# Kernel tuning notes

Hardware: AMD Instinct MI355X
Metric: run time of the kernel (lower is better)

Reference implementation:

```python
import jax, jax.numpy as jnp
import numpy as np

B, T, V, E, A, H, IMG, ENC = 128, 25, 10000, 512, 512, 512, 14, 2048
P = IMG * IMG  # 196 pixels


def setup_inputs() -> dict:
    key = jax.random.key(0)
    ks = jax.random.split(key, 24)
    w = lambda i, shape: jax.random.normal(ks[i], shape, jnp.float32) * 0.02
    captions = jax.random.randint(ks[0], (B, T), 0, V, dtype=jnp.int32)
    lens = jax.random.randint(ks[1], (B, 1), 5, T + 1, dtype=jnp.int32)
    lens = lens.at[0, 0].set(T)  # guarantee max(captions_lengths) == T (static)
    encoder_out = jax.random.normal(ks[2], (B, IMG, IMG, ENC), jnp.float32)
    return {
        'captions': captions,
        'encoder_out': encoder_out,
        'captions_lengths': lens,
        'emb_W': w(3, (V, E)),
        'att_enc_W': w(4, (A, ENC)), 'att_enc_b': jnp.zeros((A,), jnp.float32),
        'att_dec_W': w(5, (A, E)), 'att_dec_b': jnp.zeros((A,), jnp.float32),
        'att_fin_W': w(6, (1, A)), 'att_fin_b': jnp.zeros((1,), jnp.float32),
        'f_beta_W': w(7, (ENC, H)), 'f_beta_b': jnp.zeros((ENC,), jnp.float32),
        'W_ih': w(8, (4 * H, ENC + E)), 'b_ih': jnp.zeros((4 * H,), jnp.float32),
        'W_hh': w(9, (4 * H, H)), 'b_hh': jnp.zeros((4 * H,), jnp.float32),
        'lin_W': w(10, (V, H)), 'lin_b': jnp.zeros((V,), jnp.float32),
        'h_init_W': w(11, (H, ENC)), 'h_init_b': jnp.zeros((H,), jnp.float32),
        'c_init_W': w(12, (H, ENC)), 'c_init_b': jnp.zeros((H,), jnp.float32),
    }


def reference(captions, encoder_out, captions_lengths, emb_W,
              att_enc_W, att_enc_b, att_dec_W, att_dec_b, att_fin_W, att_fin_b,
              f_beta_W, f_beta_b, W_ih, b_ih, W_hh, b_hh,
              lin_W, lin_b, h_init_W, h_init_b, c_init_W, c_init_b):
    b = encoder_out.shape[0]
    enc = encoder_out.reshape(b, -1, ENC)                 # [B,P,2048]
    lens = captions_lengths[:, 0]
    sort_ind = jnp.argsort(-lens)                         # descending-length sort
    lens_s = lens[sort_ind]
    enc = enc[sort_ind]
    caps = captions[sort_ind]
    emb = emb_W[caps]                                     # [B,T,E]
    enc_mean = enc.mean(axis=1)                           # [B,2048]
    h0 = enc_mean @ h_init_W.T + h_init_b                 # [B,H]
    c0 = enc_mean @ c_init_W.T + c_init_b
    # precompute encoder side of additive attention (loop-invariant)
    att_enc = jnp.einsum('bpe,ae->bpa', enc, att_enc_W) + att_enc_b  # [B,P,A]

    t_steps = caps.shape[1]
    active = (lens_s[None, :] > jnp.arange(1, t_steps)[:, None])     # [T-1,B]
    emb_prev = jnp.swapaxes(emb[:, :t_steps - 1], 0, 1)              # [T-1,B,E]

    def step(carry, xs):
        h, c = carry
        dec, act = xs                                      # [B,E], [B]
        # additive attention
        att_d = dec @ att_dec_W.T + att_dec_b              # [B,A]
        score = jax.nn.relu(att_enc + att_d[:, None, :]) @ att_fin_W[0] + att_fin_b[0]  # [B,P]
        wts = jax.nn.softmax(score, axis=1)
        ctx = jnp.einsum('bpe,bp->be', enc, wts)           # [B,2048]
        gate = jax.nn.sigmoid(h @ f_beta_W.T + f_beta_b)   # [B,2048]
        ctx = gate * ctx
        x = jnp.concatenate([ctx, dec], axis=1)            # [B,2048+E]
        gates = x @ W_ih.T + b_ih + h @ W_hh.T + b_hh      # [B,4H]
        i, f, g, o = jnp.split(gates, 4, axis=1)
        c_new = jax.nn.sigmoid(f) * c + jax.nn.sigmoid(i) * jnp.tanh(g)
        h_new = jax.nn.sigmoid(o) * jnp.tanh(c_new)
        m = act[:, None]
        h = jnp.where(m, h_new, h)                         # finished rows frozen
        c = jnp.where(m, c_new, c)
        logits = h @ lin_W.T + lin_b                       # [B,V]
        y = jnp.where(m, logits, 0.0)                      # unwritten rows stay 0
        return (h, c), y

    (_, _), ys = jax.lax.scan(step, (h0, c0), (emb_prev, active))
    preds = jnp.zeros((b, t_steps, V), jnp.float32)
    preds = preds.at[:, 0, 0].set(1.0)
    preds = preds.at[:, 1:, :].set(jnp.swapaxes(ys, 0, 1))
    return preds, caps, lens_s, sort_ind
```

## Files before the change

### kernel.cpp

```cpp
#include <hip/hip_runtime.h>
#include <hip/hip_cooperative_groups.h>
#include <math.h>

namespace cg = cooperative_groups;

#define Bb 128
#define Tt 25
#define Vv 10000
#define Ee 512
#define Aa 512
#define Hh 512
#define ENCc 2048
#define Pp 196
#define NSTEP 24
#define NPAD 10112
#define NWG 64

#define OUT_CAPS  ((size_t)Bb*Tt*Vv)
#define OUT_LENS  (OUT_CAPS + (size_t)Bb*Tt)
#define OUT_SORT  (OUT_LENS + Bb)

typedef __bf16 bf16x8 __attribute__((ext_vector_type(8)));
typedef __bf16 bf16x4 __attribute__((ext_vector_type(4)));
typedef float  f32x4  __attribute__((ext_vector_type(4)));

__device__ __forceinline__ float sigm(float x) { return 1.0f / (1.0f + expf(-x)); }

__global__ void k_sort(const int* __restrict__ captions, const int* __restrict__ cap_lens,
                       int* sort_ind, int* lens_s, int* caps_s,
                       int* row_emb, int* logit_rowoff, int* logit_mask,
                       float* out)
{
    int b = threadIdx.x;
    __shared__ int lens_sh[Bb];
    int len = cap_lens[b];
    lens_sh[b] = len;
    __syncthreads();
    int r = 0;
    for (int k = 0; k < Bb; k++) {
        int lk = lens_sh[k];
        if (lk > len || (lk == len && k < b)) r++;
    }
    sort_ind[r] = b;
    lens_s[r] = len;
    for (int t = 0; t < Tt; t++) {
        int cv = captions[b * Tt + t];
        caps_s[r * Tt + t] = cv;
        out[OUT_CAPS + (size_t)r * Tt + t] = (float)cv;
    }
    out[OUT_LENS + r] = (float)len;
    out[OUT_SORT + r] = (float)b;
    __syncthreads();
    for (int m = b; m < NSTEP * Bb; m += Bb) {
        int t = m / Bb, bb = m % Bb;
        row_emb[m] = caps_s[bb * Tt + t];
        logit_rowoff[m] = (bb * Tt + (t + 1)) * Vv;
        logit_mask[m] = (lens_s[bb] > t + 1) ? 1 : 0;
    }
}

__global__ void k_preds0(float* out)
{
    size_t i = (size_t)blockIdx.x * 256 + threadIdx.x;
    if (i >= (size_t)Bb * Vv) return;
    size_t b = i / Vv, v = i % Vv;
    out[b * Tt * Vv + v] = (v == 0) ? 1.0f : 0.0f;
}

__global__ void k_bias(const float* b_ih, const float* b_hh,
                       const float* aeb, const float* adb,
                       float* bias2, float* bias_att)
{
    int i = blockIdx.x * 256 + threadIdx.x;
    if (i < 2048) bias2[i] = b_ih[i] + b_hh[i];
    if (i < 512)  bias_att[i] = aeb[i] + adb[i];
}

__global__ void k_cvt_enc(const float* __restrict__ src, const int* __restrict__ sind,
                          __bf16* __restrict__ dst)
{
    int row = blockIdx.y;
    int e4 = blockIdx.x * 256 + threadIdx.x;
    int b = row / Pp, p = row % Pp;
    const float4 v = *(const float4*)(src + ((size_t)(sind[b] * Pp + p)) * ENCc + e4 * 4);
    bf16x4 o = { (__bf16)v.x, (__bf16)v.y, (__bf16)v.z, (__bf16)v.w };
    *(bf16x4*)(dst + (size_t)row * ENCc + e4 * 4) = o;
}

__global__ void k_cvt(const float* __restrict__ src, __bf16* __restrict__ dst, int n4)
{
    int i = blockIdx.x * 256 + threadIdx.x;
    if (i >= n4) return;
    const float4 v = *(const float4*)(src + (size_t)i * 4);
    bf16x4 o = { (__bf16)v.x, (__bf16)v.y, (__bf16)v.z, (__bf16)v.w };
    *(bf16x4*)(dst + (size_t)i * 4) = o;
}

__global__ void k_cvt_lin(const float* __restrict__ src, __bf16* __restrict__ dst)
{
    int i = blockIdx.x * 256 + threadIdx.x;
    if (i >= NPAD * 128) return;
    int row = i >> 7, e = (i & 127) * 4;
    bf16x4 o;
    if (row < Vv) {
        const float4 v = *(const float4*)(src + (size_t)row * Hh + e);
        o = bf16x4{ (__bf16)v.x, (__bf16)v.y, (__bf16)v.z, (__bf16)v.w };
    } else {
        o = bf16x4{ (__bf16)0.f, (__bf16)0.f, (__bf16)0.f, (__bf16)0.f };
    }
    *(bf16x4*)(dst + (size_t)row * Hh + e) = o;
}

__global__ void k_cvt_emb(const float* __restrict__ emb_W, const int* __restrict__ row_emb,
                          __bf16* __restrict__ dst)
{
    int i = blockIdx.x * 256 + threadIdx.x;
    int row = i >> 7, e = (i & 127) * 4;
    const float4 v = *(const float4*)(emb_W + (size_t)row_emb[row] * Ee + e);
    bf16x4 o = { (__bf16)v.x, (__bf16)v.y, (__bf16)v.z, (__bf16)v.w };
    *(bf16x4*)(dst + (size_t)row * Ee + e) = o;
}

__global__ void k_cvt_wihd(const float* __restrict__ W_ih, __bf16* __restrict__ dst)
{
    int i = blockIdx.x * 256 + threadIdx.x;
    int row = i >> 7, e = (i & 127) * 4;
    const float4 v = *(const float4*)(W_ih + (size_t)row * 2560 + 2048 + e);
    bf16x4 o = { (__bf16)v.x, (__bf16)v.y, (__bf16)v.z, (__bf16)v.w };
    *(bf16x4*)(dst + (size_t)row * 512 + e) = o;
}

__global__ void k_wcat2(const float* __restrict__ W_ih, const float* __restrict__ W_hh,
                        __bf16* __restrict__ W2)
{
    int n = blockIdx.y;
    int k4 = blockIdx.x * 256 + threadIdx.x;
    if (k4 >= 640) return;
    int k = k4 * 4;
    float4 v;
    if (k < 2048) v = *(const float4*)(W_ih + (size_t)n * 2560 + k);
    else          v = *(const float4*)(W_hh + (size_t)n * 512 + (k - 2048));
    bf16x4 o = { (__bf16)v.x, (__bf16)v.y, (__bf16)v.z, (__bf16)v.w };
    *(bf16x4*)(W2 + (size_t)n * 2560 + k) = o;
}

__global__ void k_enc_mean(const __bf16* __restrict__ enc, __bf16* __restrict__ emean)
{
    int b = blockIdx.y;
    int e = blockIdx.x * 256 + threadIdx.x;
    const __bf16* base = enc + (size_t)b * Pp * ENCc + e;
    float s = 0.0f;
    for (int p = 0; p < Pp; p++) s += (float)base[(size_t)p * ENCc];
    emean[(size_t)b * ENCc + e] = (__bf16)(s / 196.0f);
}

template<int MODE>
__launch_bounds__(256)
__global__ void mfma_gemm(const __bf16* __restrict__ A, const __bf16* __restrict__ B,
                          const float* __restrict__ bias, void* __restrict__ Cout,
                          int K, int Nout, int Ncol,
                          const int* __restrict__ c_rowoff,
                          const int* __restrict__ mmask,
                          size_t bsA, size_t bsB, size_t bsC)
{
    __shared__ __bf16 sA[128 * 32];
    __shared__ __bf16 sB[128 * 32];
    const int tid = threadIdx.x;
    const int lane = tid & 63;
    const int wave = tid >> 6;
    const int z = blockIdx.z;
    const int m0 = blockIdx.y * 128, n0 = blockIdx.x * 128;
    const int wr = (wave & 1) * 64, wc = (wave >> 1) * 64;
    f32x4 acc[4][4] = {};
    const __bf16* Aptr = A + bsA * z + (size_t)m0 * K;
    const __bf16* Bptr = B + bsB * z + (size_t)n0 * K;
    const int c0 = tid, c1 = tid + 256;
    const int ar0 = c0 >> 2, ak0 = (c0 & 3) * 8;
    const int ar1 = c1 >> 2, ak1 = (c1 & 3) * 8;
    const int kq = (lane >> 4) * 8, mr = lane & 15;

    for (int k0 = 0; k0 < K; k0 += 32) {
        __builtin_amdgcn_global_load_lds(
            (const __attribute__((address_space(1))) void*)(Aptr + (size_t)ar0 * K + k0 + ak0),
            (__attribute__((address_space(3))) void*)(sA + c0 * 8), 16, 0, 0);
        __builtin_amdgcn_global_load_lds(
            (const __attribute__((address_space(1))) void*)(Aptr + (size_t)ar1 * K + k0 + ak1),
            (__attribute__((address_space(3))) void*)(sA + c1 * 8), 16, 0, 0);
        __builtin_amdgcn_global_load_lds(
            (const __attribute__((address_space(1))) void*)(Bptr + (size_t)ar0 * K + k0 + ak0),
            (__attribute__((address_space(3))) void*)(sB + c0 * 8), 16, 0, 0);
        __builtin_amdgcn_global_load_lds(
            (const __attribute__((address_space(1))) void*)(Bptr + (size_t)ar1 * K + k0 + ak1),
            (__attribute__((address_space(3))) void*)(sB + c1 * 8), 16, 0, 0);
        __syncthreads();
        bf16x8 af[4], bfr[4];
        #pragma unroll
        for (int i = 0; i < 4; i++)
            af[i] = *(const bf16x8*)(sA + (wr + i * 16 + mr) * 32 + kq);
        #pragma unroll
        for (int j = 0; j < 4; j++)
            bfr[j] = *(const bf16x8*)(sB + (wc + j * 16 + mr) * 32 + kq);
        #pragma unroll
        for (int i = 0; i < 4; i++)
            #pragma unroll
            for (int j = 0; j < 4; j++)
                acc[i][j] = __builtin_amdgcn_mfma_f32_16x16x32_bf16(af[i], bfr[j], acc[i][j], 0, 0, 0);
        __syncthreads();
    }

    const int rq = (lane >> 4) * 4, cq = lane & 15;
    #pragma unroll
    for (int i = 0; i < 4; i++) {
        #pragma unroll
        for (int j = 0; j < 4; j++) {
            #pragma unroll
            for (int r = 0; r < 4; r++) {
                int row = m0 + wr + i * 16 + rq + r;
                int col = n0 + wc + j * 16 + cq;
                if ((MODE == 1 || MODE == 2) && col >= Ncol) continue;
                float v = acc[i][j][r] + (bias ? bias[col] : 0.0f);
                size_t ro = (c_rowoff ? (size_t)c_rowoff[row] : (size_t)row * Nout) + bsC * z;
                if (MODE == 2) {
                    if (!mmask[row]) v = 0.0f;
                    ((float*)Cout)[ro + col] = v;
                } else if (MODE == 1) {
                    ((__bf16*)Cout)[ro + col] = (__bf16)v;
                } else {
                    ((float*)Cout)[ro + col] = v;
                }
            }
        }
    }
}

__global__ void k_scores(const __bf16* __restrict__ ET, const float* __restrict__ att_d,
                         const float* __restrict__ fin_W, const float* __restrict__ fin_b,
                         float* __restrict__ wts)
{
    __shared__ float Dls[512 * 12];
    const int b = blockIdx.y;
    const int tb = blockIdx.x * 12;
    const int tid = threadIdx.x;
    #pragma unroll
    for (int tt = 0; tt < 12; tt++)
        for (int a = tid; a < 512; a += 256)
            Dls[a * 12 + tt] = att_d[((size_t)(tb + tt) * Bb + b) * Aa + a];
    __syncthreads();
    const int p = tid;
    if (p >= Pp) return;
    float acc[12];
    #pragma unroll
    for (int i = 0; i < 12; i++) acc[i] = 0.0f;
    const __bf16* ep = ET + (size_t)b * Aa * Pp + p;
    for (int a = 0; a < 512; a++) {
        float e = (float)ep[(size_t)a * Pp];
        float fw = fin_W[a];
        const float4* dp = (const float4*)(Dls + a * 12);
        float4 d0 = dp[0], d1 = dp[1], d2 = dp[2];
        acc[0] += fmaxf(e + d0.x, 0.0f) * fw;
        acc[1] += fmaxf(e + d0.y, 0.0f) * fw;
        acc[2] += fmaxf(e + d0.z, 0.0f) * fw;
        acc[3] += fmaxf(e + d0.w, 0.0f) * fw;
        acc[4] += fmaxf(e + d1.x, 0.0f) * fw;
        acc[5] += fmaxf(e + d1.y, 0.0f) * fw;
        acc[6] += fmaxf(e + d1.z, 0.0f) * fw;
        acc[7] += fmaxf(e + d1.w, 0.0f) * fw;
        acc[8] += fmaxf(e + d2.x, 0.0f) * fw;
        acc[9] += fmaxf(e + d2.y, 0.0f) * fw;
        acc[10] += fmaxf(e + d2.z, 0.0f) * fw;
        acc[11] += fmaxf(e + d2.w, 0.0f) * fw;
    }
    float fb = fin_b[0];
    #pragma unroll
    for (int tt = 0; tt < 12; tt++)
        wts[((size_t)(tb + tt) * Bb + b) * Pp + p] = acc[tt] + fb;
}

__global__ void k_softmax(float* scores)
{
    int tb = blockIdx.x;
    float* row = scores + (size_t)tb * Pp;
    int lane = threadIdx.x;
    float v[4];
    float mx = -1e30f;
    #pragma unroll
    for (int i = 0; i < 4; i++) {
        int p = lane + i * 64;
        v[i] = (p < Pp) ? row[p] : -1e30f;
        mx = fmaxf(mx, v[i]);
    }
    #pragma unroll
    for (int off = 32; off > 0; off >>= 1) mx = fmaxf(mx, __shfl_down(mx, off));
    mx = __shfl(mx, 0);
    float s = 0.0f;
    #pragma unroll
    for (int i = 0; i < 4; i++) {
        int p = lane + i * 64;
        v[i] = (p < Pp) ? expf(v[i] - mx) : 0.0f;
        s += v[i];
    }
    #pragma unroll
    for (int off = 32; off > 0; off >>= 1) s += __shfl_down(s, off);
    s = __shfl(s, 0);
    float inv = 1.0f / s;
    #pragma unroll
    for (int i = 0; i < 4; i++) {
        int p = lane + i * 64;
        if (p < Pp) row[p] = v[i] * inv;
    }
}

__global__ void k_ctx(const __bf16* __restrict__ enc, const float* __restrict__ wts,
                      float* __restrict__ ctx_raw)
{
    int b = blockIdx.y;
    int e = blockIdx.x * 256 + threadIdx.x;
    __shared__ float w_s[NSTEP][Pp];
    int tid = threadIdx.x;
    for (int idx = tid; idx < NSTEP * Pp; idx += 256) {
        int t = idx / Pp, p = idx % Pp;
        w_s[t][p] = wts[((size_t)t * Bb + b) * Pp + p];
    }
    __syncthreads();
    const __bf16* base = enc + (size_t)b * Pp * ENCc + e;
    float acc[NSTEP];
    #pragma unroll
    for (int t = 0; t < NSTEP; t++) acc[t] = 0.0f;
    for (int p = 0; p < Pp; p++) {
        float v = (float)base[(size_t)p * ENCc];
        #pragma unroll
        for (int t = 0; t < NSTEP; t++) acc[t] += w_s[t][p] * v;
    }
    for (int t = 0; t < NSTEP; t++)
        ctx_raw[((size_t)t * Bb + b) * ENCc + e] = acc[t];
}

__device__ __forceinline__ bf16x8 lds_frag(const __bf16* s, int row, int g)
{
    int slot = row * 16 + (g ^ (row & 7));
    return *(const bf16x8*)(s + slot * 8);
}

__launch_bounds__(256)
__global__ void k_loop(__bf16* __restrict__ xctx, __bf16* __restrict__ hbuf0,
                       __bf16* __restrict__ hbuf1, float* __restrict__ cbuf,
                       const float* __restrict__ ctx_raw,
                       const __bf16* __restrict__ fbW, const float* __restrict__ fbb,
                       const __bf16* __restrict__ W2, const float* __restrict__ gdec,
                       __bf16* __restrict__ hall, const int* __restrict__ lens)
{
    cg::grid_group grid = cg::this_grid();
    __shared__ __bf16 sA[128 * 128];
    __shared__ __bf16 sB[32 * 128];
    const int tid = threadIdx.x, lane = tid & 63, wave = tid >> 6;
    const int wg = blockIdx.x;
    const int cq = lane & 15, rq4 = (lane >> 4) * 4;
    const int mbase = wave * 32;
    const int kq = lane >> 4;

    for (int t = 0; t < NSTEP; t++) {
        const __bf16* hcur = (t & 1) ? hbuf1 : hbuf0;
        __bf16* hnext = (t & 1) ? hbuf0 : hbuf1;
        {
            const int cb = wg * 32;
            f32x4 acc[2][2] = {};
            for (int k0 = 0; k0 < 512; k0 += 128) {
                #pragma unroll
                for (int i = 0; i < 8; i++) {
                    int flat = tid + 256 * i;
                    int row = flat >> 4, gs = flat & 15;
                    int gsrc = gs ^ (row & 7);
                    __builtin_amdgcn_global_load_lds(
                        (const __attribute__((address_space(1))) void*)(hcur + (size_t)row * 512 + k0 + gsrc * 8),
                        (__attribute__((address_space(3))) void*)(sA + flat * 8), 16, 0, 0);
                }
                #pragma unroll
                for (int i = 0; i < 2; i++) {
                    int flat = tid + 256 * i;
                    int row = flat >> 4, gs = flat & 15;
                    int gsrc = gs ^ (row & 7);
                    __builtin_amdgcn_global_load_lds(
                        (const __attribute__((address_space(1))) void*)(fbW + (size_t)(cb + row) * 512 + k0 + gsrc * 8),
                        (__attribute__((address_space(3))) void*)(sB + flat * 8), 16, 0, 0);
                }
                __syncthreads();
                #pragma unroll
                for (int ks = 0; ks < 4; ks++) {
                    int g = ks * 4 + kq;
                    bf16x8 af[2], bfv[2];
                    #pragma unroll
                    for (int mi = 0; mi < 2; mi++) af[mi] = lds_frag(sA, mbase + mi * 16 + cq, g);
                    #pragma unroll
                    for (int ni = 0; ni < 2; ni++) bfv[ni] = lds_frag(sB, ni * 16 + cq, g);
                    #pragma unroll
                    for (int mi = 0; mi < 2; mi++)
                        #pragma unroll
                        for (int ni = 0; ni < 2; ni++)
                            acc[mi][ni] = __builtin_amdgcn_mfma_f32_16x16x32_bf16(af[mi], bfv[ni], acc[mi][ni], 0, 0, 0);
                }
                __syncthreads();
            }
            const float* cr = ctx_raw + (size_t)t * Bb * ENCc;
            #pragma unroll
            for (int mi = 0; mi < 2; mi++)
                #pragma unroll
                for (int ni = 0; ni < 2; ni++)
                    #pragma unroll
                    for (int r = 0; r < 4; r++) {
                        int row = mbase + mi * 16 + rq4 + r;
                        int col = cb + ni * 16 + cq;
                        float v = acc[mi][ni][r] + fbb[col];
                        float x = sigm(v) * cr[(size_t)row * ENCc + col];
                        xctx[(size_t)row * ENCc + col] = (__bf16)x;
                    }
        }
        grid.sync();
        {
            const int jb = wg * 8;
            f32x4 acc[2][2] = {};
            for (int k0 = 0; k0 < 2560; k0 += 128) {
                const bool inH = (k0 >= 2048);
                #pragma unroll
                for (int i = 0; i < 8; i++) {
                    int flat = tid + 256 * i;
                    int row = flat >> 4, gs = flat & 15;
                    int gsrc = gs ^ (row & 7);
                    const __bf16* src = inH ? (hcur + (size_t)row * 512 + (k0 - 2048) + gsrc * 8)
                                            : (xctx + (size_t)row * ENCc + k0 + gsrc * 8);
                    __builtin_amdgcn_global_load_lds(
                        (const __attribute__((address_space(1))) void*)src,
                        (__attribute__((address_space(3))) void*)(sA + flat * 8), 16, 0, 0);
                }
                #pragma unroll
                for (int i = 0; i < 2; i++) {
                    int flat = tid + 256 * i;
                    int row = flat >> 4, gs = flat & 15;
                    int gsrc = gs ^ (row & 7);
                    int wrow = (row >> 3) * 512 + jb + (row & 7);
                    __builtin_amdgcn_global_load_lds(
                        (const __attribute__((address_space(1))) void*)(W2 + (size_t)wrow * 2560 + k0 + gsrc * 8),
                        (__attribute__((address_space(3))) void*)(sB + flat * 8), 16, 0, 0);
                }
                __syncthreads();
                #pragma unroll
                for (int ks = 0; ks < 4; ks++) {
                    int g = ks * 4 + kq;
                    bf16x8 af[2], bfv[2];
                    #pragma unroll
                    for (int mi = 0; mi < 2; mi++) af[mi] = lds_frag(sA, mbase + mi * 16 + cq, g);
                    #pragma unroll
                    for (int ni = 0; ni < 2; ni++) bfv[ni] = lds_frag(sB, ni * 16 + cq, g);
                    #pragma unroll
                    for (int mi = 0; mi < 2; mi++)
                        #pragma unroll
                        for (int ni = 0; ni < 2; ni++)
                            acc[mi][ni] = __builtin_amdgcn_mfma_f32_16x16x32_bf16(af[mi], bfv[ni], acc[mi][ni], 0, 0, 0);
                }
                __syncthreads();
            }
            const int j = jb + (cq & 7);
            const int g0 = cq >> 3;
            #pragma unroll
            for (int mi = 0; mi < 2; mi++)
                #pragma unroll
                for (int r = 0; r < 4; r++) {
                    int row = mbase + mi * 16 + rq4 + r;
                    size_t gb = (size_t)(t * Bb + row) * 2048;
                    float a0 = acc[mi][0][r] + gdec[gb + (size_t)g0 * 512 + j];
                    float a1 = acc[mi][1][r] + gdec[gb + (size_t)(2 + g0) * 512 + j];
                    float p0 = __shfl_xor(a0, 8);
                    float p1 = __shfl_xor(a1, 8);
                    float iv, fv, gv, ov;
                    if (cq < 8) { iv = a0; gv = a1; fv = p0; ov = p1; }
                    else        { iv = p0; gv = p1; fv = a0; ov = a1; }
                    float co = cbuf[(size_t)row * 512 + j];
                    float cn = sigm(fv) * co + sigm(iv) * tanhf(gv);
                    float hn = sigm(ov) * tanhf(cn);
                    bool act = lens[row] > (t + 1);
                    __bf16 hold = hcur[(size_t)row * 512 + j];
                    __bf16 hv = act ? (__bf16)hn : hold;
                    if (cq < 8) {
                        if (act) cbuf[(size_t)row * 512 + j] = cn;
                        hnext[(size_t)row * 512 + j] = hv;
                        hall[((size_t)t * Bb + row) * 512 + j] = hv;
                    }
                }
        }
        grid.sync();
    }
}

extern "C" void kernel_launch(void* const* d_in, const int* in_sizes, int n_in,
                              void* d_out, int out_size, void* d_ws, size_t ws_size,
                              hipStream_t stream)
{
    const int*   captions    = (const int*)d_in[0];
    const float* encoder_out = (const float*)d_in[1];
    const int*   cap_lens    = (const int*)d_in[2];
    const float* emb_W       = (const float*)d_in[3];
    const float* att_enc_W   = (const float*)d_in[4];
    const float* att_enc_b   = (const float*)d_in[5];
    const float* att_dec_W   = (const float*)d_in[6];
    const float* att_dec_b   = (const float*)d_in[7];
    const float* att_fin_W   = (const float*)d_in[8];
    const float* att_fin_b   = (const float*)d_in[9];
    const float* f_beta_W    = (const float*)d_in[10];
    const float* f_beta_b    = (const float*)d_in[11];
    const float* W_ih        = (const float*)d_in[12];
    const float* b_ih        = (const float*)d_in[13];
    const float* W_hh        = (const float*)d_in[14];
    const float* b_hh        = (const float*)d_in[15];
    const float* lin_W       = (const float*)d_in[16];
    const float* lin_b       = (const float*)d_in[17];
    const float* h_init_W    = (const float*)d_in[18];
    const float* h_init_b    = (const float*)d_in[19];
    const float* c_init_W    = (const float*)d_in[20];
    const float* c_init_b    = (const float*)d_in[21];
    float* out = (float*)d_out;

    float* f = (float*)d_ws;
    float* ctx_raw  = f; f += (size_t)NSTEP * Bb * ENCc;
    float* att_d    = f; f += (size_t)NSTEP * Bb * Aa;
    float* wts      = f; f += (size_t)NSTEP * Bb * Pp;
    float* cbuf     = f; f += (size_t)Bb * Hh;
    float* gdec     = f; f += (size_t)NSTEP * Bb * 2048;
    float* bias2    = f; f += 2048;
    float* bias_att = f; f += 512;
    __bf16* bp = (__bf16*)f;
    __bf16* enc_s = bp; bp += (size_t)Bb * Pp * ENCc + 131072;
    __bf16* ET    = bp; bp += (size_t)Bb * Aa * Pp;
    __bf16* attW  = bp; bp += (size_t)Aa * ENCc;
    __bf16* attdW = bp; bp += (size_t)Aa * Ee;
    __bf16* fbW   = bp; bp += (size_t)ENCc * Hh;
    __bf16* hiW   = bp; bp += (size_t)Hh * ENCc;
    __bf16* ciW   = bp; bp += (size_t)Hh * ENCc;
    __bf16* linWb = bp; bp += (size_t)NPAD * Hh;
    __bf16* embg  = bp; bp += (size_t)NSTEP * Bb * Ee;
    __bf16* hall  = bp; bp += (size_t)NSTEP * Bb * Hh;
    __bf16* hbuf0 = bp; bp += (size_t)Bb * Hh;
    __bf16* hbuf1 = bp; bp += (size_t)Bb * Hh;
    __bf16* emean = bp; bp += (size_t)Bb * ENCc;
    __bf16* W2    = bp; bp += (size_t)2048 * 2560;
    __bf16* Wihd  = bp; bp += (size_t)2048 * 512;
    __bf16* xctx  = bp; bp += (size_t)Bb * ENCc;
    int* ip = (int*)bp;
    int* sort_ind     = ip; ip += Bb;
    int* lens_s       = ip; ip += Bb;
    int* caps_s       = ip; ip += Bb * Tt;
    int* row_emb      = ip; ip += NSTEP * Bb;
    int* logit_rowoff = ip; ip += NSTEP * Bb;
    int* logit_mask   = ip; ip += NSTEP * Bb;

    k_sort<<<1, Bb, 0, stream>>>(captions, cap_lens, sort_ind, lens_s, caps_s,
                                 row_emb, logit_rowoff, logit_mask, out);
    k_preds0<<<(Bb * Vv + 255) / 256, 256, 0, stream>>>(out);
    k_bias<<<8, 256, 0, stream>>>(b_ih, b_hh, att_enc_b, att_dec_b, bias2, bias_att);
    k_cvt_enc<<<dim3(2, Bb * Pp), 256, 0, stream>>>(encoder_out, sort_ind, enc_s);
    k_cvt<<<(Aa * ENCc / 4 + 255) / 256, 256, 0, stream>>>(att_enc_W, attW, Aa * ENCc / 4);
    k_cvt<<<(Aa * Ee / 4 + 255) / 256, 256, 0, stream>>>(att_dec_W, attdW, Aa * Ee / 4);
    k_cvt<<<(ENCc * Hh / 4 + 255) / 256, 256, 0, stream>>>(f_beta_W, fbW, ENCc * Hh / 4);
    k_cvt<<<(Hh * ENCc / 4 + 255) / 256, 256, 0, stream>>>(h_init_W, hiW, Hh * ENCc / 4);
    k_cvt<<<(Hh * ENCc / 4 + 255) / 256, 256, 0, stream>>>(c_init_W, ciW, Hh * ENCc / 4);
    k_cvt_lin<<<(NPAD * 128 + 255) / 256, 256, 0, stream>>>(lin_W, linWb);
    k_cvt_emb<<<(NSTEP * Bb * 128) / 256, 256, 0, stream>>>(emb_W, row_emb, embg);
    k_cvt_wihd<<<(2048 * 128) / 256, 256, 0, stream>>>(W_ih, Wihd);
    k_wcat2<<<dim3(3, 2048), 256, 0, stream>>>(W_ih, W_hh, W2);
    k_enc_mean<<<dim3(ENCc / 256, Bb), 256, 0, stream>>>(enc_s, emean);
    mfma_gemm<1><<<dim3(4, 1), 256, 0, stream>>>(emean, hiW, h_init_b, hbuf0,
        ENCc, Hh, 512, nullptr, nullptr, 0, 0, 0);
    mfma_gemm<0><<<dim3(4, 1), 256, 0, stream>>>(emean, ciW, c_init_b, cbuf,
        ENCc, Hh, 512, nullptr, nullptr, 0, 0, 0);
    mfma_gemm<1><<<dim3(2, 4, Bb), 256, 0, stream>>>(attW, enc_s, nullptr, ET,
        ENCc, Pp, Pp, nullptr, nullptr, 0, (size_t)Pp * ENCc, (size_t)Aa * Pp);
    mfma_gemm<0><<<dim3(4, NSTEP * Bb / 128), 256, 0, stream>>>(embg, attdW, bias_att, att_d,
        Ee, Aa, 512, nullptr, nullptr, 0, 0, 0);
    mfma_gemm<0><<<dim3(16, NSTEP * Bb / 128), 256, 0, stream>>>(embg, Wihd, bias2, gdec,
        Ee, 2048, 2048, nullptr, nullptr, 0, 0, 0);
    k_scores<<<dim3(2, Bb), 256, 0, stream>>>(ET, att_d, att_fin_W, att_fin_b, wts);
    k_softmax<<<NSTEP * Bb, 64, 0, stream>>>(wts);
    k_ctx<<<dim3(ENCc / 256, Bb), 256, 0, stream>>>(enc_s, wts, ctx_raw);
    {
        void* args[] = { &xctx, &hbuf0, &hbuf1, &cbuf, &ctx_raw, &fbW,
                         (void*)&f_beta_b, &W2, &gdec, &hall, &lens_s };
        hipLaunchCooperativeKernel((void*)k_loop, dim3(NWG), dim3(256), args, 0, stream);
    }
    mfma_gemm<2><<<dim3(NPAD / 128, NSTEP * Bb / 128), 256, 0, stream>>>(hall, linWb, lin_b, out,
        Hh, 0, Vv, logit_rowoff, logit_mask, 0, 0, 0);
}
```

Baseline: 2.267 ms.

## Keep recurrent weights register-resident across steps with split-K waves and more workgroups

The persistent LSTM loop kernel now loads each workgroup's slice of the f_beta and combined LSTM weights into registers once, before the time loop. Previously those weights were streamed through LDS on every step. Each of the four waves handles a quarter of the K dimension, reading activations straight from global memory, and partial sums are reduced through LDS. The grid doubles to 128 workgroups, so each one owns fewer output columns. This removes repeated weight traffic and per-tile LDS staging barriers, at the cost of heavy register use, uncoalesced direct activation loads, and grid syncs across more workgroups.

```diff
diff --git a/kernel.cpp b/kernel.cpp
--- a/kernel.cpp
+++ b/kernel.cpp
@@ -14,7 +14,7 @@
 #define Pp 196
 #define NSTEP 24
 #define NPAD 10112
-#define NWG 64
+#define NWG 128
 
 #define OUT_CAPS  ((size_t)Bb*Tt*Vv)
 #define OUT_LENS  (OUT_CAPS + (size_t)Bb*Tt)
@@ -335,13 +335,7 @@
         ctx_raw[((size_t)t * Bb + b) * ENCc + e] = acc[t];
 }
 
-__device__ __forceinline__ bf16x8 lds_frag(const __bf16* s, int row, int g)
-{
-    int slot = row * 16 + (g ^ (row & 7));
-    return *(const bf16x8*)(s + slot * 8);
-}
-
-__launch_bounds__(256)
+__launch_bounds__(256, 1)
 __global__ void k_loop(__bf16* __restrict__ xctx, __bf16* __restrict__ hbuf0,
                        __bf16* __restrict__ hbuf1, float* __restrict__ cbuf,
                        const float* __restrict__ ctx_raw,
@@ -350,141 +344,123 @@
                        __bf16* __restrict__ hall, const int* __restrict__ lens)
 {
     cg::grid_group grid = cg::this_grid();
-    __shared__ __bf16 sA[128 * 128];
-    __shared__ __bf16 sB[32 * 128];
-    const int tid = threadIdx.x, lane = tid & 63, wave = tid >> 6;
+    __shared__ f32x4 red[4][8][64];
+    const int tid = threadIdx.x, lane = tid & 63, w = tid >> 6;
     const int wg = blockIdx.x;
-    const int cq = lane & 15, rq4 = (lane >> 4) * 4;
-    const int mbase = wave * 32;
-    const int kq = lane >> 4;
+    const int cl = lane & 15;
+    const int koff = (lane >> 4) * 8;
+    const int rq4 = (lane >> 4) * 4;
+    const int cq = cl;
+    const int jb4 = wg * 4;
+    const int cb = wg * 16;
+
+    bf16x8 w2f[20];
+    bf16x8 fbA[4];
+    {
+        const int Rrow = (cl >> 2) * 512 + jb4 + (cl & 3);
+        #pragma unroll
+        for (int jj = 0; jj < 20; jj++) {
+            int ks = w * 20 + jj;
+            w2f[jj] = *(const bf16x8*)(W2 + (size_t)Rrow * 2560 + ks * 32 + koff);
+        }
+        #pragma unroll
+        for (int jj = 0; jj < 4; jj++) {
+            int ks = w * 4 + jj;
+            fbA[jj] = *(const bf16x8*)(fbW + (size_t)(cb + cl) * 512 + ks * 32 + koff);
+        }
+    }
 
     for (int t = 0; t < NSTEP; t++) {
         const __bf16* hcur = (t & 1) ? hbuf1 : hbuf0;
         __bf16* hnext = (t & 1) ? hbuf0 : hbuf1;
+
         {
-            const int cb = wg * 32;
-            f32x4 acc[2][2] = {};
-            for (int k0 = 0; k0 < 512; k0 += 128) {
+            f32x4 acc[8] = {};
+            #pragma unroll
+            for (int jj = 0; jj < 4; jj++) {
+                const __bf16* Ab = hcur + (w * 4 + jj) * 32 + koff;
+                bf16x8 a[8];
                 #pragma unroll
-                for (int i = 0; i < 8; i++) {
-                    int flat = tid + 256 * i;
-                    int row = flat >> 4, gs = flat & 15;
-                    int gsrc = gs ^ (row & 7);
-                    __builtin_amdgcn_global_load_lds(
-                        (const __attribute__((address_space(1))) void*)(hcur + (size_t)row * 512 + k0 + gsrc * 8),
-                        (__attribute__((address_space(3))) void*)(sA + flat * 8), 16, 0, 0);
+                for (int m = 0; m < 8; m++)
+                    a[m] = *(const bf16x8*)(Ab + (size_t)(m * 16 + cl) * 512);
+                #pragma unroll
+                for (int m = 0; m < 8; m++)
+                    acc[m] = __builtin_amdgcn_mfma_f32_16x16x32_bf16(a[m], fbA[jj], acc[m], 0, 0, 0);
+            }
+            #pragma unroll
+            for (int m = 0; m < 8; m++) red[w][m][lane] = acc[m];
+            __syncthreads();
+            const float* cr = ctx_raw + (size_t)t * Bb * ENCc;
+            #pragma unroll
+            for (int mi = 0; mi < 2; mi++) {
+                int m = w * 2 + mi;
+                f32x4 s0 = red[0][m][lane], s1 = red[1][m][lane];
+                f32x4 s2 = red[2][m][lane], s3 = red[3][m][lane];
+                int col = cb + cq;
+                float fb = fbb[col];
+                #pragma unroll
+                for (int r = 0; r < 4; r++) {
+                    int row = m * 16 + rq4 + r;
+                    float v = s0[r] + s1[r] + s2[r] + s3[r] + fb;
+                    float x = sigm(v) * cr[(size_t)row * ENCc + col];
+                    xctx[(size_t)row * ENCc + col] = (__bf16)x;
                 }
-                #pragma unroll
-                for (int i = 0; i < 2; i++) {
-                    int flat = tid + 256 * i;
-                    int row = flat >> 4, gs = flat & 15;
-                    int gsrc = gs ^ (row & 7);
-                    __builtin_amdgcn_global_load_lds(
-                        (const __attribute__((address_space(1))) void*)(fbW + (size_t)(cb + row) * 512 + k0 + gsrc * 8),
-                        (__attribute__((address_space(3))) void*)(sB + flat * 8), 16, 0, 0);
-                }
-                __syncthreads();
-                #pragma unroll
-                for (int ks = 0; ks < 4; ks++) {
-                    int g = ks * 4 + kq;
-                    bf16x8 af[2], bfv[2];
-                    #pragma unroll
-                    for (int mi = 0; mi < 2; mi++) af[mi] = lds_frag(sA, mbase + mi * 16 + cq, g);
-                    #pragma unroll
-                    for (int ni = 0; ni < 2; ni++) bfv[ni] = lds_frag(sB, ni * 16 + cq, g);
-                    #pragma unroll
-                    for (int mi = 0; mi < 2; mi++)
-                        #pragma unroll
-                        for (int ni = 0; ni < 2; ni++)
-                            acc[mi][ni] = __builtin_amdgcn_mfma_f32_16x16x32_bf16(af[mi], bfv[ni], acc[mi][ni], 0, 0, 0);
-                }
-                __syncthreads();
             }
-            const float* cr = ctx_raw + (size_t)t * Bb * ENCc;
-            #pragma unroll
-            for (int mi = 0; mi < 2; mi++)
-                #pragma unroll
-                for (int ni = 0; ni < 2; ni++)
-                    #pragma unroll
-                    for (int r = 0; r < 4; r++) {
-                        int row = mbase + mi * 16 + rq4 + r;
-                        int col = cb + ni * 16 + cq;
-                        float v = acc[mi][ni][r] + fbb[col];
-                        float x = sigm(v) * cr[(size_t)row * ENCc + col];
-                        xctx[(size_t)row * ENCc + col] = (__bf16)x;
-                    }
         }
         grid.sync();
+
         {
-            const int jb = wg * 8;
-            f32x4 acc[2][2] = {};
-            for (int k0 = 0; k0 < 2560; k0 += 128) {
-                const bool inH = (k0 >= 2048);
+            f32x4 acc[8] = {};
+            #pragma unroll
+            for (int jj = 0; jj < 20; jj++) {
+                const int ks = w * 20 + jj;
+                const __bf16* Ab;
+                int stride;
+                if (ks < 64) { Ab = xctx + ks * 32 + koff; stride = ENCc; }
+                else         { Ab = hcur + (ks - 64) * 32 + koff; stride = 512; }
+                bf16x8 a[8];
                 #pragma unroll
-                for (int i = 0; i < 8; i++) {
-                    int flat = tid + 256 * i;
-                    int row = flat >> 4, gs = flat & 15;
-                    int gsrc = gs ^ (row & 7);
-                    const __bf16* src = inH ? (hcur + (size_t)row * 512 + (k0 - 2048) + gsrc * 8)
-                                            : (xctx + (size_t)row * ENCc + k0 + gsrc * 8);
-                    __builtin_amdgcn_global_load_lds(
-                        (const __attribute__((address_space(1))) void*)src,
-                        (__attribute__((address_space(3))) void*)(sA + flat * 8), 16, 0, 0);
-                }
+                for (int m = 0; m < 8; m++)
+                    a[m] = *(const bf16x8*)(Ab + (size_t)(m * 16 + cl) * stride);
                 #pragma unroll
-                for (int i = 0; i < 2; i++) {
-                    int flat = tid + 256 * i;
-                    int row = flat >> 4, gs = flat & 15;
-                    int gsrc = gs ^ (row & 7);
-                    int wrow = (row >> 3) * 512 + jb + (row & 7);
-                    __builtin_amdgcn_global_load_lds(
-                        (const __attribute__((address_space(1))) void*)(W2 + (size_t)wrow * 2560 + k0 + gsrc * 8),
-                        (__attribute__((address_space(3))) void*)(sB + flat * 8), 16, 0, 0);
-                }
-                __syncthreads();
-                #pragma unroll
-                for (int ks = 0; ks < 4; ks++) {
-                    int g = ks * 4 + kq;
-                    bf16x8 af[2], bfv[2];
-                    #pragma unroll
-                    for (int mi = 0; mi < 2; mi++) af[mi] = lds_frag(sA, mbase + mi * 16 + cq, g);
-                    #pragma unroll
-                    for (int ni = 0; ni < 2; ni++) bfv[ni] = lds_frag(sB, ni * 16 + cq, g);
-                    #pragma unroll
-                    for (int mi = 0; mi < 2; mi++)
-                        #pragma unroll
-                        for (int ni = 0; ni < 2; ni++)
-                            acc[mi][ni] = __builtin_amdgcn_mfma_f32_16x16x32_bf16(af[mi], bfv[ni], acc[mi][ni], 0, 0, 0);
-                }
-                __syncthreads();
+                for (int m = 0; m < 8; m++)
+                    acc[m] = __builtin_amdgcn_mfma_f32_16x16x32_bf16(a[m], w2f[jj], acc[m], 0, 0, 0);
             }
-            const int j = jb + (cq & 7);
-            const int g0 = cq >> 3;
-            #pragma unroll
-            for (int mi = 0; mi < 2; mi++)
+            #pragma unroll
+            for (int m = 0; m < 8; m++) red[w][m][lane] = acc[m];
+            __syncthreads();
+            const int gi = cq >> 2;
+            const int jo = cq & 3;
+            const int j = jb4 + jo;
+            const int basel = lane & 48;
+            const float* gd = gdec + (size_t)t * Bb * 2048;
+            #pragma unroll
+            for (int mi = 0; mi < 2; mi++) {
+                int m = w * 2 + mi;
+                f32x4 s0 = red[0][m][lane], s1 = red[1][m][lane];
+                f32x4 s2 = red[2][m][lane], s3 = red[3][m][lane];
                 #pragma unroll
                 for (int r = 0; r < 4; r++) {
-                    int row = mbase + mi * 16 + rq4 + r;
-                    size_t gb = (size_t)(t * Bb + row) * 2048;
-                    float a0 = acc[mi][0][r] + gdec[gb + (size_t)g0 * 512 + j];
-                    float a1 = acc[mi][1][r] + gdec[gb + (size_t)(2 + g0) * 512 + j];
-                    float p0 = __shfl_xor(a0, 8);
-                    float p1 = __shfl_xor(a1, 8);
-                    float iv, fv, gv, ov;
-                    if (cq < 8) { iv = a0; gv = a1; fv = p0; ov = p1; }
-                    else        { iv = p0; gv = p1; fv = a0; ov = a1; }
+                    int row = m * 16 + rq4 + r;
+                    float aval = s0[r] + s1[r] + s2[r] + s3[r]
+                               + gd[(size_t)row * 2048 + gi * 512 + j];
+                    float iv = __shfl(aval, basel | (0  + jo), 64);
+                    float fv = __shfl(aval, basel | (4  + jo), 64);
+                    float gv = __shfl(aval, basel | (8  + jo), 64);
+                    float ov = __shfl(aval, basel | (12 + jo), 64);
                     float co = cbuf[(size_t)row * 512 + j];
                     float cn = sigm(fv) * co + sigm(iv) * tanhf(gv);
                     float hn = sigm(ov) * tanhf(cn);
                     bool act = lens[row] > (t + 1);
                     __bf16 hold = hcur[(size_t)row * 512 + j];
                     __bf16 hv = act ? (__bf16)hn : hold;
-                    if (cq < 8) {
+                    if (cq < 4) {
                         if (act) cbuf[(size_t)row * 512 + j] = cn;
                         hnext[(size_t)row * 512 + j] = hv;
                         hall[((size_t)t * Bb + row) * 512 + j] = hv;
                     }
                 }
+            }
         }
         grid.sync();
     }
```

Measured after the change: 2.688 ms. 1.19x slower.
